# Performance work log

Measured on AMD Instinct MI355X. Metric: run time of the kernel, lower is better.

The kernel has to match this reference:

```python
import jax, jax.numpy as jnp
import numpy as np

F_DIM, P_DIM, H_DIM, N_EXP = 768, 512, 1024, 4
B, T = 8192, 8192


def _gelu(x):
    return jax.nn.gelu(x, approximate=False)


def _normalize(x, eps=1e-12):
    n = jnp.linalg.norm(x, axis=-1, keepdims=True)
    return x / jnp.maximum(n, eps)


def setup_inputs() -> dict:
    key = jax.random.key(0)
    ks = jax.random.split(key, 24)
    s = 0.02
    inp = {
        'image_features': jax.random.normal(ks[0], (B, F_DIM), jnp.float32),
        'text_features': jax.random.normal(ks[1], (B, F_DIM), jnp.float32),
        'target_features': jax.random.normal(ks[2], (T, F_DIM), jnp.float32),
        # projection layers (torch Linear convention: W [out,in])
        'Wt': jax.random.normal(ks[3], (P_DIM, F_DIM), jnp.float32) * s,
        'bt': jnp.zeros((P_DIM,), jnp.float32),
        'Wi': jax.random.normal(ks[4], (P_DIM, F_DIM), jnp.float32) * s,
        'bi': jnp.zeros((P_DIM,), jnp.float32),
        # dynamic scalar MLP: (2P -> H -> 1)
        'ds_W1': jax.random.normal(ks[5], (H_DIM, 2 * P_DIM), jnp.float32) * s,
        'ds_b1': jnp.zeros((H_DIM,), jnp.float32),
        'ds_W2': jax.random.normal(ks[6], (1, H_DIM), jnp.float32) * s,
        'ds_b2': jnp.zeros((1,), jnp.float32),
        # experts stacked: [E, H, 2P]
        'exp_W': jax.random.normal(ks[7], (N_EXP, H_DIM, 2 * P_DIM), jnp.float32) * s,
        'exp_b': jnp.zeros((N_EXP, H_DIM), jnp.float32),
        # router: (2P -> H/4 -> E)
        'rt_W1': jax.random.normal(ks[8], (H_DIM // 4, 2 * P_DIM), jnp.float32) * s,
        'rt_b1': jnp.zeros((H_DIM // 4,), jnp.float32),
        'rt_W2': jax.random.normal(ks[9], (N_EXP, H_DIM // 4), jnp.float32) * s,
        'rt_b2': jnp.zeros((N_EXP,), jnp.float32),
        # output layer: (H -> F)
        'out_W': jax.random.normal(ks[10], (F_DIM, H_DIM), jnp.float32) * s,
        'out_b': jnp.zeros((F_DIM,), jnp.float32),
        'logit_scale': jnp.asarray(np.log(50.0), jnp.float32),
    }
    return inp


def reference(image_features, text_features, target_features, Wt, bt, Wi, bi,
              ds_W1, ds_b1, ds_W2, ds_b2, exp_W, exp_b,
              rt_W1, rt_b1, rt_W2, rt_b2, out_W, out_b, logit_scale):
    # eval mode: all dropouts are identity, no modality drop
    tp = _gelu(text_features @ Wt.T + bt)            # [B,P]
    ip = _gelu(image_features @ Wi.T + bi)           # [B,P]
    comb = jnp.concatenate([tp, ip], axis=-1)        # [B,2P]

    router_logits = _gelu(comb @ rt_W1.T + rt_b1) @ rt_W2.T + rt_b2  # [B,E]
    router_probs = jax.nn.softmax(router_logits, axis=-1)

    expert_out = _gelu(jnp.einsum('bd,ehd->beh', comb, exp_W) + exp_b)  # [B,E,H]
    fused_hidden = jnp.einsum('be,beh->bh', router_probs, expert_out)   # [B,H]
    residual = fused_hidden @ out_W.T + out_b                            # [B,F]

    ds = jax.nn.sigmoid(_gelu(comb @ ds_W1.T + ds_b1) @ ds_W2.T + ds_b2)  # [B,1]
    output = ds * text_features + (1.0 - ds) * image_features + residual
    pred = _normalize(output)
    tgt = _normalize(target_features)
    logits = jnp.exp(logit_scale) * (pred @ tgt.T)   # [B,T]
    return (logits, ds, router_probs)
```

## Files before the change

### kernel.cpp

```cpp
#include <hip/hip_runtime.h>
#include <stdint.h>
#include <math.h>

#define BDIM 8192
#define TDIM 8192
#define FDIM 768
#define PDIM 512
#define HDIM 1024
#define NEXP 4
#define NCAT 5376

using short8 = __attribute__((ext_vector_type(8))) short;
using f32x4  = __attribute__((ext_vector_type(4))) float;

__device__ __forceinline__ short f2bf(float f) {
  uint32_t u = __builtin_bit_cast(uint32_t, f);
  u += 0x7fffu + ((u >> 16) & 1u);
  return (short)(u >> 16);
}
__device__ __forceinline__ float bf2f(short s) {
  uint32_t u = ((uint32_t)(uint16_t)s) << 16;
  return __builtin_bit_cast(float, u);
}
__device__ __forceinline__ float gelu_exact(float x) {
  return 0.5f * x * (1.0f + erff(x * 0.70710678118654752f));
}

#define GLDS(gp, lp) __builtin_amdgcn_global_load_lds( \
    (const __attribute__((address_space(1))) void*)(gp), \
    (__attribute__((address_space(3))) void*)(lp), 16, 0, 0)

template <int MODE>
__global__ __launch_bounds__(256, 2)
void gemm_bt(const short* __restrict__ A, int lda,
             const short* __restrict__ B, int ldb,
             void* __restrict__ C, int ldc, int K,
             const float* __restrict__ bias,
             const float* __restrict__ scale_ptr)
{
  __shared__ short sA[4096];
  __shared__ short sB[4096];
  const int t    = threadIdx.x;
  const int lane = t & 63;
  const int wave = t >> 6;
  const int m0 = blockIdx.y * 128;
  const int n0 = blockIdx.x * 128;
  const int wm = (wave >> 1) * 64;
  const int wn = (wave & 1) * 64;
  const int l15  = lane & 15;
  const int quad = lane >> 4;

  f32x4 acc[4][4];
#pragma unroll
  for (int i = 0; i < 4; ++i)
#pragma unroll
    for (int j = 0; j < 4; ++j)
      acc[i][j] = (f32x4){0.f, 0.f, 0.f, 0.f};

  const int rr = t >> 2;
  const int cc = (t & 3) * 8;
  const short* gA0 = A + (size_t)(m0 + rr) * lda + cc;
  const short* gA1 = A + (size_t)(m0 + 64 + rr) * lda + cc;
  const short* gB0 = B + (size_t)(n0 + rr) * ldb + cc;
  const short* gB1 = B + (size_t)(n0 + 64 + rr) * ldb + cc;
  short* lA0 = sA + t * 8;
  short* lA1 = sA + 2048 + t * 8;
  short* lB0 = sB + t * 8;
  short* lB1 = sB + 2048 + t * 8;

  for (int k0 = 0; k0 < K; k0 += 32) {
    GLDS(gA0 + k0, lA0);
    GLDS(gA1 + k0, lA1);
    GLDS(gB0 + k0, lB0);
    GLDS(gB1 + k0, lB1);
    __syncthreads();
    short8 af[4], bfr[4];
#pragma unroll
    for (int i = 0; i < 4; ++i)
      af[i] = *(const short8*)(sA + (wm + i * 16 + l15) * 32 + quad * 8);
#pragma unroll
    for (int j = 0; j < 4; ++j)
      bfr[j] = *(const short8*)(sB + (wn + j * 16 + l15) * 32 + quad * 8);
#pragma unroll
    for (int i = 0; i < 4; ++i)
#pragma unroll
      for (int j = 0; j < 4; ++j)
        acc[i][j] = __builtin_amdgcn_mfma_f32_16x16x32_bf16(af[i], bfr[j], acc[i][j], 0, 0, 0);
    __syncthreads();
  }

  float scale = 1.f;
  if (MODE == 2) scale = expf(scale_ptr[0]);
#pragma unroll
  for (int i = 0; i < 4; ++i) {
#pragma unroll
    for (int j = 0; j < 4; ++j) {
      const int col = n0 + wn + j * 16 + l15;
      float bv = (MODE == 2) ? 0.f : bias[col];
#pragma unroll
      for (int r = 0; r < 4; ++r) {
        const int row = m0 + wm + i * 16 + quad * 4 + r;
        float v = acc[i][j][r];
        if (MODE == 0) {
          v = gelu_exact(v + bv);
          ((short*)C)[(size_t)row * ldc + col] = f2bf(v);
        } else if (MODE == 1) {
          ((float*)C)[(size_t)row * ldc + col] = v + bv;
        } else {
          ((float*)C)[(size_t)row * ldc + col] = v * scale;
        }
      }
    }
  }
}

__global__ __launch_bounds__(256)
void f32_to_bf16(const float* __restrict__ src, short* __restrict__ dst, int n) {
  int i = blockIdx.x * 256 + threadIdx.x;
  if (i < n) dst[i] = f2bf(src[i]);
}

__global__ __launch_bounds__(256)
void concat_bias(const float* __restrict__ exp_b, const float* __restrict__ ds_b1,
                 const float* __restrict__ rt_b1, float* __restrict__ bias_cat) {
  int i = blockIdx.x * 256 + threadIdx.x;
  if (i >= NCAT) return;
  float v;
  if (i < 4096)      v = exp_b[i];
  else if (i < 5120) v = ds_b1[i - 4096];
  else               v = rt_b1[i - 5120];
  bias_cat[i] = v;
}

__global__ __launch_bounds__(256)
void router_ds(const short* __restrict__ Hall,
               const float* __restrict__ rt_W2, const float* __restrict__ rt_b2,
               const float* __restrict__ ds_W2, const float* __restrict__ ds_b2,
               float* __restrict__ out_probs, float* __restrict__ out_ds)
{
  const int row  = blockIdx.x * 4 + (threadIdx.x >> 6);
  const int lane = threadIdx.x & 63;
  const short* h = Hall + (size_t)row * NCAT;
  float s0 = 0, s1 = 0, s2 = 0, s3 = 0, d = 0;
  for (int i = lane; i < 256; i += 64) {
    float v = bf2f(h[5120 + i]);
    s0 += v * rt_W2[i];
    s1 += v * rt_W2[256 + i];
    s2 += v * rt_W2[512 + i];
    s3 += v * rt_W2[768 + i];
  }
  for (int i = lane; i < 1024; i += 64)
    d += bf2f(h[4096 + i]) * ds_W2[i];
#pragma unroll
  for (int off = 32; off; off >>= 1) {
    s0 += __shfl_xor(s0, off);
    s1 += __shfl_xor(s1, off);
    s2 += __shfl_xor(s2, off);
    s3 += __shfl_xor(s3, off);
    d  += __shfl_xor(d, off);
  }
  if (lane == 0) {
    float l0 = s0 + rt_b2[0], l1 = s1 + rt_b2[1];
    float l2 = s2 + rt_b2[2], l3 = s3 + rt_b2[3];
    float mx = fmaxf(fmaxf(l0, l1), fmaxf(l2, l3));
    float e0 = expf(l0 - mx), e1 = expf(l1 - mx);
    float e2 = expf(l2 - mx), e3 = expf(l3 - mx);
    float inv = 1.f / (e0 + e1 + e2 + e3);
    out_probs[row * 4 + 0] = e0 * inv;
    out_probs[row * 4 + 1] = e1 * inv;
    out_probs[row * 4 + 2] = e2 * inv;
    out_probs[row * 4 + 3] = e3 * inv;
    out_ds[row] = 1.f / (1.f + expf(-(d + ds_b2[0])));
  }
}

__global__ __launch_bounds__(256)
void fuse_experts(const short* __restrict__ Hall, const float* __restrict__ probs,
                  short* __restrict__ fused)
{
  const int idx  = blockIdx.x * 256 + threadIdx.x;
  const int b    = idx >> 10;
  const int hcol = idx & 1023;
  const short* hb = Hall + (size_t)b * NCAT;
  const float* p  = probs + (size_t)b * 4;
  float v = p[0] * bf2f(hb[hcol])        + p[1] * bf2f(hb[1024 + hcol])
          + p[2] * bf2f(hb[2048 + hcol]) + p[3] * bf2f(hb[3072 + hcol]);
  fused[idx] = f2bf(v);
}

__global__ __launch_bounds__(256)
void combine_normalize(const float* __restrict__ text, const float* __restrict__ image,
                       const float* __restrict__ ds, const float* __restrict__ src,
                       short* __restrict__ dst)
{
  const int b = blockIdx.x;
  const int t = threadIdx.x;
  const float* s = src + (size_t)b * FDIM;
  float o0, o1, o2;
  if (text != nullptr) {
    const float dv = ds[b];
    const float* tx = text + (size_t)b * FDIM;
    const float* im = image + (size_t)b * FDIM;
    o0 = dv * tx[t]       + (1.f - dv) * im[t]       + s[t];
    o1 = dv * tx[t + 256] + (1.f - dv) * im[t + 256] + s[t + 256];
    o2 = dv * tx[t + 512] + (1.f - dv) * im[t + 512] + s[t + 512];
  } else {
    o0 = s[t]; o1 = s[t + 256]; o2 = s[t + 512];
  }
  float ss = o0 * o0 + o1 * o1 + o2 * o2;
  __shared__ float red[4];
#pragma unroll
  for (int off = 32; off; off >>= 1) ss += __shfl_xor(ss, off);
  if ((t & 63) == 0) red[t >> 6] = ss;
  __syncthreads();
  const float tot = red[0] + red[1] + red[2] + red[3];
  const float rn = 1.f / fmaxf(sqrtf(tot), 1e-12f);
  short* d = dst + (size_t)b * FDIM;
  d[t]       = f2bf(o0 * rn);
  d[t + 256] = f2bf(o1 * rn);
  d[t + 512] = f2bf(o2 * rn);
}

extern "C" void kernel_launch(void* const* d_in, const int* in_sizes, int n_in,
                              void* d_out, int out_size, void* d_ws, size_t ws_size,
                              hipStream_t stream) {
  const float* image  = (const float*)d_in[0];
  const float* text   = (const float*)d_in[1];
  const float* target = (const float*)d_in[2];
  const float* Wt     = (const float*)d_in[3];
  const float* bt     = (const float*)d_in[4];
  const float* Wi     = (const float*)d_in[5];
  const float* bi     = (const float*)d_in[6];
  const float* ds_W1  = (const float*)d_in[7];
  const float* ds_b1  = (const float*)d_in[8];
  const float* ds_W2  = (const float*)d_in[9];
  const float* ds_b2  = (const float*)d_in[10];
  const float* exp_W  = (const float*)d_in[11];
  const float* exp_b  = (const float*)d_in[12];
  const float* rt_W1  = (const float*)d_in[13];
  const float* rt_b1  = (const float*)d_in[14];
  const float* rt_W2  = (const float*)d_in[15];
  const float* rt_b2  = (const float*)d_in[16];
  const float* out_W  = (const float*)d_in[17];
  const float* out_b  = (const float*)d_in[18];
  const float* logit_scale = (const float*)d_in[19];

  char* ws = (char*)d_ws;
  short* comb  = (short*)ws;  ws += (size_t)BDIM * 1024 * 2;
  short* Hall  = (short*)ws;  ws += (size_t)BDIM * NCAT * 2;
  short* fused = (short*)ws;  ws += (size_t)BDIM * 1024 * 2;
  float* resid = (float*)ws;  ws += (size_t)BDIM * FDIM * 4;
  short* pred  = (short*)ws;  ws += (size_t)BDIM * FDIM * 2;
  short* tgtb  = (short*)ws;  ws += (size_t)TDIM * FDIM * 2;
  short* textb = (short*)ws;  ws += (size_t)BDIM * FDIM * 2;
  short* imgb  = (short*)ws;  ws += (size_t)BDIM * FDIM * 2;
  short* Wtb   = (short*)ws;  ws += (size_t)PDIM * FDIM * 2;
  short* Wib   = (short*)ws;  ws += (size_t)PDIM * FDIM * 2;
  short* outWb = (short*)ws;  ws += (size_t)FDIM * HDIM * 2;
  short* Bcat  = (short*)ws;  ws += (size_t)NCAT * HDIM * 2;
  float* biascat = (float*)ws; ws += (size_t)NCAT * 4;

  float* out_logits = (float*)d_out;
  float* out_ds     = out_logits + (size_t)BDIM * TDIM;
  float* out_probs  = out_ds + BDIM;

  {
    int n;
    n = BDIM * FDIM;  f32_to_bf16<<<(n + 255) / 256, 256, 0, stream>>>(text,  textb, n);
    n = BDIM * FDIM;  f32_to_bf16<<<(n + 255) / 256, 256, 0, stream>>>(image, imgb,  n);
    n = PDIM * FDIM;  f32_to_bf16<<<(n + 255) / 256, 256, 0, stream>>>(Wt,    Wtb,   n);
    n = PDIM * FDIM;  f32_to_bf16<<<(n + 255) / 256, 256, 0, stream>>>(Wi,    Wib,   n);
    n = NEXP * HDIM * 1024; f32_to_bf16<<<(n + 255) / 256, 256, 0, stream>>>(exp_W, Bcat, n);
    n = HDIM * 1024;  f32_to_bf16<<<(n + 255) / 256, 256, 0, stream>>>(ds_W1, Bcat + (size_t)4096 * 1024, n);
    n = 256 * 1024;   f32_to_bf16<<<(n + 255) / 256, 256, 0, stream>>>(rt_W1, Bcat + (size_t)5120 * 1024, n);
    n = FDIM * HDIM;  f32_to_bf16<<<(n + 255) / 256, 256, 0, stream>>>(out_W, outWb, n);
    concat_bias<<<(NCAT + 255) / 256, 256, 0, stream>>>(exp_b, ds_b1, rt_b1, biascat);
  }

  dim3 blk(256);
  gemm_bt<0><<<dim3(PDIM / 128, BDIM / 128), blk, 0, stream>>>(textb, FDIM, Wtb, FDIM, comb,        1024, FDIM, bt, nullptr);
  gemm_bt<0><<<dim3(PDIM / 128, BDIM / 128), blk, 0, stream>>>(imgb,  FDIM, Wib, FDIM, comb + 512,  1024, FDIM, bi, nullptr);
  gemm_bt<0><<<dim3(NCAT / 128, BDIM / 128), blk, 0, stream>>>(comb, 1024, Bcat, 1024, Hall, NCAT, 1024, biascat, nullptr);
  router_ds<<<BDIM / 4, 256, 0, stream>>>(Hall, rt_W2, rt_b2, ds_W2, ds_b2, out_probs, out_ds);
  fuse_experts<<<(BDIM * HDIM) / 256, 256, 0, stream>>>(Hall, out_probs, fused);
  gemm_bt<1><<<dim3(FDIM / 128, BDIM / 128), blk, 0, stream>>>(fused, 1024, outWb, 1024, resid, FDIM, 1024, out_b, nullptr);
  combine_normalize<<<BDIM, 256, 0, stream>>>(text, image, out_ds, resid, pred);
  combine_normalize<<<TDIM, 256, 0, stream>>>(nullptr, nullptr, nullptr, target, tgtb);
  gemm_bt<2><<<dim3(TDIM / 128, BDIM / 128), blk, 0, stream>>>(pred, FDIM, tgtb, FDIM, out_logits, TDIM, FDIM, nullptr, logit_scale);
}
```

Before: 734.4 us.

## Merge prep conversions, projection GEMMs, router+expert mix, and normalizations into fewer launches

```diff
diff --git a/kernel.cpp b/kernel.cpp
--- a/kernel.cpp
+++ b/kernel.cpp
@@ -10,6 +10,7 @@
 #define NEXP 4
 #define NCAT 5376
 
+using short4v = __attribute__((ext_vector_type(4))) short;
 using short8 = __attribute__((ext_vector_type(8))) short;
 using f32x4  = __attribute__((ext_vector_type(4))) float;
 
@@ -31,20 +32,18 @@
     (__attribute__((address_space(3))) void*)(lp), 16, 0, 0)
 
 template <int MODE>
-__global__ __launch_bounds__(256, 2)
-void gemm_bt(const short* __restrict__ A, int lda,
-             const short* __restrict__ B, int ldb,
-             void* __restrict__ C, int ldc, int K,
-             const float* __restrict__ bias,
-             const float* __restrict__ scale_ptr)
+__device__ __forceinline__ void gemm_body(
+    const short* __restrict__ A, int lda,
+    const short* __restrict__ B, int ldb,
+    void* __restrict__ C, int ldc, int K,
+    const float* __restrict__ bias, float scale,
+    int m0, int n0)
 {
   __shared__ short sA[4096];
   __shared__ short sB[4096];
   const int t    = threadIdx.x;
   const int lane = t & 63;
   const int wave = t >> 6;
-  const int m0 = blockIdx.y * 128;
-  const int n0 = blockIdx.x * 128;
   const int wm = (wave >> 1) * 64;
   const int wn = (wave & 1) * 64;
   const int l15  = lane & 15;
@@ -89,8 +88,6 @@
     __syncthreads();
   }
 
-  float scale = 1.f;
-  if (MODE == 2) scale = expf(scale_ptr[0]);
 #pragma unroll
   for (int i = 0; i < 4; ++i) {
 #pragma unroll
@@ -114,98 +111,184 @@
   }
 }
 
+template <int MODE>
+__global__ __launch_bounds__(256, 2)
+void gemm_bt(const short* __restrict__ A, int lda,
+             const short* __restrict__ B, int ldb,
+             void* __restrict__ C, int ldc, int K,
+             const float* __restrict__ bias,
+             const float* __restrict__ scale_ptr)
+{
+  float scale = 1.f;
+  if (MODE == 2) scale = expf(scale_ptr[0]);
+  gemm_body<MODE>(A, lda, B, ldb, C, ldc, K, bias, scale,
+                  blockIdx.y * 128, blockIdx.x * 128);
+}
+
+__global__ __launch_bounds__(256, 2)
+void gemm_proj(const short* __restrict__ textb, const short* __restrict__ imgb,
+               const short* __restrict__ Wtb, const short* __restrict__ Wib,
+               const float* __restrict__ bt, const float* __restrict__ bi,
+               short* __restrict__ comb)
+{
+  const int z = blockIdx.z;
+  const short* A = z ? imgb : textb;
+  const short* B = z ? Wib : Wtb;
+  const float* bias = z ? bi : bt;
+  short* C = comb + (z ? 512 : 0);
+  gemm_body<0>(A, FDIM, B, FDIM, C, 1024, FDIM, bias, 1.f,
+               blockIdx.y * 128, blockIdx.x * 128);
+}
+
+#define SEG0 1572864u
+#define SEG1 3145728u
+#define SEG2 3244032u
+#define SEG3 3342336u
+#define SEG4 4390912u
+#define SEG5 4653056u
+#define SEG6 4718592u
+#define SEG7 4915200u
+#define SEG8 4916544u
+
 __global__ __launch_bounds__(256)
-void f32_to_bf16(const float* __restrict__ src, short* __restrict__ dst, int n) {
-  int i = blockIdx.x * 256 + threadIdx.x;
-  if (i < n) dst[i] = f2bf(src[i]);
+void prep_all(const float* __restrict__ text, const float* __restrict__ image,
+              const float* __restrict__ Wt, const float* __restrict__ Wi,
+              const float* __restrict__ exp_W, const float* __restrict__ ds_W1,
+              const float* __restrict__ rt_W1, const float* __restrict__ out_W,
+              const float* __restrict__ exp_b, const float* __restrict__ ds_b1,
+              const float* __restrict__ rt_b1,
+              short* __restrict__ textb, short* __restrict__ imgb,
+              short* __restrict__ Wtb, short* __restrict__ Wib,
+              short* __restrict__ Bcat, short* __restrict__ outWb,
+              float* __restrict__ biascat)
+{
+  const uint32_t i = blockIdx.x * 256 + threadIdx.x;
+  if (i >= SEG8) return;
+  if (i >= SEG7) {
+    const uint32_t j = (i - SEG7) * 4;
+#pragma unroll
+    for (int k = 0; k < 4; ++k) {
+      uint32_t idx = j + k;
+      float v;
+      if (idx < 4096)      v = exp_b[idx];
+      else if (idx < 5120) v = ds_b1[idx - 4096];
+      else                 v = rt_b1[idx - 5120];
+      biascat[idx] = v;
+    }
+    return;
+  }
+  const float* s;
+  short* d;
+  uint32_t j;
+  if (i < SEG1) {
+    if (i < SEG0) { j = i;        s = text;  d = textb; }
+    else          { j = i - SEG0; s = image; d = imgb;  }
+  } else if (i < SEG3) {
+    if (i < SEG2) { j = i - SEG1; s = Wt; d = Wtb; }
+    else          { j = i - SEG2; s = Wi; d = Wib; }
+  } else if (i < SEG5) {
+    if (i < SEG4) { j = i - SEG3; s = exp_W; d = Bcat; }
+    else          { j = i - SEG4; s = ds_W1; d = Bcat + (size_t)4096 * 1024; }
+  } else {
+    if (i < SEG6) { j = i - SEG5; s = rt_W1; d = Bcat + (size_t)5120 * 1024; }
+    else          { j = i - SEG6; s = out_W; d = outWb; }
+  }
+  float4 v = ((const float4*)s)[j];
+  short4v o = { f2bf(v.x), f2bf(v.y), f2bf(v.z), f2bf(v.w) };
+  ((short4v*)d)[j] = o;
 }
 
 __global__ __launch_bounds__(256)
-void concat_bias(const float* __restrict__ exp_b, const float* __restrict__ ds_b1,
-                 const float* __restrict__ rt_b1, float* __restrict__ bias_cat) {
-  int i = blockIdx.x * 256 + threadIdx.x;
-  if (i >= NCAT) return;
-  float v;
-  if (i < 4096)      v = exp_b[i];
-  else if (i < 5120) v = ds_b1[i - 4096];
-  else               v = rt_b1[i - 5120];
-  bias_cat[i] = v;
-}
-
-__global__ __launch_bounds__(256)
-void router_ds(const short* __restrict__ Hall,
-               const float* __restrict__ rt_W2, const float* __restrict__ rt_b2,
-               const float* __restrict__ ds_W2, const float* __restrict__ ds_b2,
-               float* __restrict__ out_probs, float* __restrict__ out_ds)
-{
-  const int row  = blockIdx.x * 4 + (threadIdx.x >> 6);
-  const int lane = threadIdx.x & 63;
-  const short* h = Hall + (size_t)row * NCAT;
-  float s0 = 0, s1 = 0, s2 = 0, s3 = 0, d = 0;
-  for (int i = lane; i < 256; i += 64) {
-    float v = bf2f(h[5120 + i]);
-    s0 += v * rt_W2[i];
-    s1 += v * rt_W2[256 + i];
-    s2 += v * rt_W2[512 + i];
-    s3 += v * rt_W2[768 + i];
-  }
-  for (int i = lane; i < 1024; i += 64)
-    d += bf2f(h[4096 + i]) * ds_W2[i];
+void moe_mix(const short* __restrict__ Hall,
+             const float* __restrict__ rt_W2, const float* __restrict__ rt_b2,
+             const float* __restrict__ ds_W2, const float* __restrict__ ds_b2,
+             float* __restrict__ out_probs, float* __restrict__ out_ds,
+             short* __restrict__ fused)
+{
+  const int b = blockIdx.x;
+  const int t = threadIdx.x;
+  const int lane = t & 63;
+  const int wave = t >> 6;
+  const short* h = Hall + (size_t)b * NCAT;
+
+  float rv = bf2f(h[5120 + t]);
+  float p0 = rv * rt_W2[t];
+  float p1 = rv * rt_W2[256 + t];
+  float p2 = rv * rt_W2[512 + t];
+  float p3 = rv * rt_W2[768 + t];
+  float dd = 0.f;
+#pragma unroll
+  for (int k = 0; k < 4; ++k)
+    dd += bf2f(h[4096 + k * 256 + t]) * ds_W2[k * 256 + t];
+
 #pragma unroll
   for (int off = 32; off; off >>= 1) {
-    s0 += __shfl_xor(s0, off);
-    s1 += __shfl_xor(s1, off);
-    s2 += __shfl_xor(s2, off);
-    s3 += __shfl_xor(s3, off);
-    d  += __shfl_xor(d, off);
-  }
+    p0 += __shfl_xor(p0, off);
+    p1 += __shfl_xor(p1, off);
+    p2 += __shfl_xor(p2, off);
+    p3 += __shfl_xor(p3, off);
+    dd += __shfl_xor(dd, off);
+  }
+  __shared__ float red[5][4];
+  __shared__ float bc[5];
   if (lane == 0) {
-    float l0 = s0 + rt_b2[0], l1 = s1 + rt_b2[1];
-    float l2 = s2 + rt_b2[2], l3 = s3 + rt_b2[3];
+    red[0][wave] = p0; red[1][wave] = p1; red[2][wave] = p2;
+    red[3][wave] = p3; red[4][wave] = dd;
+  }
+  __syncthreads();
+  if (t == 0) {
+    float l0 = red[0][0] + red[0][1] + red[0][2] + red[0][3] + rt_b2[0];
+    float l1 = red[1][0] + red[1][1] + red[1][2] + red[1][3] + rt_b2[1];
+    float l2 = red[2][0] + red[2][1] + red[2][2] + red[2][3] + rt_b2[2];
+    float l3 = red[3][0] + red[3][1] + red[3][2] + red[3][3] + rt_b2[3];
+    float d  = red[4][0] + red[4][1] + red[4][2] + red[4][3] + ds_b2[0];
     float mx = fmaxf(fmaxf(l0, l1), fmaxf(l2, l3));
     float e0 = expf(l0 - mx), e1 = expf(l1 - mx);
     float e2 = expf(l2 - mx), e3 = expf(l3 - mx);
     float inv = 1.f / (e0 + e1 + e2 + e3);
-    out_probs[row * 4 + 0] = e0 * inv;
-    out_probs[row * 4 + 1] = e1 * inv;
-    out_probs[row * 4 + 2] = e2 * inv;
-    out_probs[row * 4 + 3] = e3 * inv;
-    out_ds[row] = 1.f / (1.f + expf(-(d + ds_b2[0])));
+    bc[0] = e0 * inv; bc[1] = e1 * inv; bc[2] = e2 * inv; bc[3] = e3 * inv;
+    bc[4] = 1.f / (1.f + expf(-d));
+    out_probs[b * 4 + 0] = bc[0];
+    out_probs[b * 4 + 1] = bc[1];
+    out_probs[b * 4 + 2] = bc[2];
+    out_probs[b * 4 + 3] = bc[3];
+    out_ds[b] = bc[4];
+  }
+  __syncthreads();
+  const float q0 = bc[0], q1 = bc[1], q2 = bc[2], q3 = bc[3];
+  short* fr = fused + (size_t)b * 1024;
+#pragma unroll
+  for (int c = t; c < 1024; c += 256) {
+    float v = q0 * bf2f(h[c])        + q1 * bf2f(h[1024 + c])
+            + q2 * bf2f(h[2048 + c]) + q3 * bf2f(h[3072 + c]);
+    fr[c] = f2bf(v);
   }
 }
 
 __global__ __launch_bounds__(256)
-void fuse_experts(const short* __restrict__ Hall, const float* __restrict__ probs,
-                  short* __restrict__ fused)
-{
-  const int idx  = blockIdx.x * 256 + threadIdx.x;
-  const int b    = idx >> 10;
-  const int hcol = idx & 1023;
-  const short* hb = Hall + (size_t)b * NCAT;
-  const float* p  = probs + (size_t)b * 4;
-  float v = p[0] * bf2f(hb[hcol])        + p[1] * bf2f(hb[1024 + hcol])
-          + p[2] * bf2f(hb[2048 + hcol]) + p[3] * bf2f(hb[3072 + hcol]);
-  fused[idx] = f2bf(v);
-}
-
-__global__ __launch_bounds__(256)
-void combine_normalize(const float* __restrict__ text, const float* __restrict__ image,
-                       const float* __restrict__ ds, const float* __restrict__ src,
-                       short* __restrict__ dst)
-{
-  const int b = blockIdx.x;
+void normalize_both(const float* __restrict__ text, const float* __restrict__ image,
+                    const float* __restrict__ ds, const float* __restrict__ resid,
+                    const float* __restrict__ target,
+                    short* __restrict__ pred, short* __restrict__ tgtb)
+{
+  const int bb = blockIdx.x;
   const int t = threadIdx.x;
-  const float* s = src + (size_t)b * FDIM;
   float o0, o1, o2;
-  if (text != nullptr) {
-    const float dv = ds[b];
-    const float* tx = text + (size_t)b * FDIM;
-    const float* im = image + (size_t)b * FDIM;
+  short* d;
+  if (bb < BDIM) {
+    const float dv = ds[bb];
+    const float* tx = text + (size_t)bb * FDIM;
+    const float* im = image + (size_t)bb * FDIM;
+    const float* s  = resid + (size_t)bb * FDIM;
     o0 = dv * tx[t]       + (1.f - dv) * im[t]       + s[t];
     o1 = dv * tx[t + 256] + (1.f - dv) * im[t + 256] + s[t + 256];
     o2 = dv * tx[t + 512] + (1.f - dv) * im[t + 512] + s[t + 512];
+    d = pred + (size_t)bb * FDIM;
   } else {
+    const int b = bb - BDIM;
+    const float* s = target + (size_t)b * FDIM;
     o0 = s[t]; o1 = s[t + 256]; o2 = s[t + 512];
+    d = tgtb + (size_t)b * FDIM;
   }
   float ss = o0 * o0 + o1 * o1 + o2 * o2;
   __shared__ float red[4];
@@ -215,7 +298,6 @@
   __syncthreads();
   const float tot = red[0] + red[1] + red[2] + red[3];
   const float rn = 1.f / fmaxf(sqrtf(tot), 1e-12f);
-  short* d = dst + (size_t)b * FDIM;
   d[t]       = f2bf(o0 * rn);
   d[t + 256] = f2bf(o1 * rn);
   d[t + 512] = f2bf(o2 * rn);
@@ -264,27 +346,22 @@
   float* out_ds     = out_logits + (size_t)BDIM * TDIM;
   float* out_probs  = out_ds + BDIM;
 
-  {
-    int n;
-    n = BDIM * FDIM;  f32_to_bf16<<<(n + 255) / 256, 256, 0, stream>>>(text,  textb, n);
-    n = BDIM * FDIM;  f32_to_bf16<<<(n + 255) / 256, 256, 0, stream>>>(image, imgb,  n);
-    n = PDIM * FDIM;  f32_to_bf16<<<(n + 255) / 256, 256, 0, stream>>>(Wt,    Wtb,   n);
-    n = PDIM * FDIM;  f32_to_bf16<<<(n + 255) / 256, 256, 0, stream>>>(Wi,    Wib,   n);
-    n = NEXP * HDIM * 1024; f32_to_bf16<<<(n + 255) / 256, 256, 0, stream>>>(exp_W, Bcat, n);
-    n = HDIM * 1024;  f32_to_bf16<<<(n + 255) / 256, 256, 0, stream>>>(ds_W1, Bcat + (size_t)4096 * 1024, n);
-    n = 256 * 1024;   f32_to_bf16<<<(n + 255) / 256, 256, 0, stream>>>(rt_W1, Bcat + (size_t)5120 * 1024, n);
-    n = FDIM * HDIM;  f32_to_bf16<<<(n + 255) / 256, 256, 0, stream>>>(out_W, outWb, n);
-    concat_bias<<<(NCAT + 255) / 256, 256, 0, stream>>>(exp_b, ds_b1, rt_b1, biascat);
-  }
+  prep_all<<<(SEG8 + 255) / 256, 256, 0, stream>>>(
+      text, image, Wt, Wi, exp_W, ds_W1, rt_W1, out_W,
+      exp_b, ds_b1, rt_b1,
+      textb, imgb, Wtb, Wib, Bcat, outWb, biascat);
 
   dim3 blk(256);
-  gemm_bt<0><<<dim3(PDIM / 128, BDIM / 128), blk, 0, stream>>>(textb, FDIM, Wtb, FDIM, comb,        1024, FDIM, bt, nullptr);
-  gemm_bt<0><<<dim3(PDIM / 128, BDIM / 128), blk, 0, stream>>>(imgb,  FDIM, Wib, FDIM, comb + 512,  1024, FDIM, bi, nullptr);
-  gemm_bt<0><<<dim3(NCAT / 128, BDIM / 128), blk, 0, stream>>>(comb, 1024, Bcat, 1024, Hall, NCAT, 1024, biascat, nullptr);
-  router_ds<<<BDIM / 4, 256, 0, stream>>>(Hall, rt_W2, rt_b2, ds_W2, ds_b2, out_probs, out_ds);
-  fuse_experts<<<(BDIM * HDIM) / 256, 256, 0, stream>>>(Hall, out_probs, fused);
-  gemm_bt<1><<<dim3(FDIM / 128, BDIM / 128), blk, 0, stream>>>(fused, 1024, outWb, 1024, resid, FDIM, 1024, out_b, nullptr);
-  combine_normalize<<<BDIM, 256, 0, stream>>>(text, image, out_ds, resid, pred);
-  combine_normalize<<<TDIM, 256, 0, stream>>>(nullptr, nullptr, nullptr, target, tgtb);
-  gemm_bt<2><<<dim3(TDIM / 128, BDIM / 128), blk, 0, stream>>>(pred, FDIM, tgtb, FDIM, out_logits, TDIM, FDIM, nullptr, logit_scale);
-}
+  gemm_proj<<<dim3(PDIM / 128, BDIM / 128, 2), blk, 0, stream>>>(
+      textb, imgb, Wtb, Wib, bt, bi, comb);
+  gemm_bt<0><<<dim3(NCAT / 128, BDIM / 128), blk, 0, stream>>>(
+      comb, 1024, Bcat, 1024, Hall, NCAT, 1024, biascat, nullptr);
+  moe_mix<<<BDIM, 256, 0, stream>>>(Hall, rt_W2, rt_b2, ds_W2, ds_b2,
+                                    out_probs, out_ds, fused);
+  gemm_bt<1><<<dim3(FDIM / 128, BDIM / 128), blk, 0, stream>>>(
+      fused, 1024, outWb, 1024, resid, FDIM, 1024, out_b, nullptr);
+  normalize_both<<<BDIM + TDIM, 256, 0, stream>>>(
+      text, image, out_ds, resid, target, pred, tgtb);
+  gemm_bt<2><<<dim3(TDIM / 128, BDIM / 128), blk, 0, stream>>>(
+      pred, FDIM, tgtb, FDIM, out_logits, TDIM, FDIM, nullptr, logit_scale);
+}
```

Result: faster. 667.2 us (-9.1%).
